# Performance work log

Hardware: AMD Instinct MI355X
Metric: run time of the kernel (lower is better)

## Reference

```python
import jax, jax.numpy as jnp
import numpy as np

INV_SQRT2 = 0.7071067811865476  # 1/sqrt(2), Haar / bior1.1 coefficient


def setup_inputs() -> dict:
    key = jax.random.key(0)
    ks = jax.random.split(key, 4)
    B, C, L = 8, 256, 4096
    s = 1.0 / np.sqrt(C).astype(np.float32)  # conv1d-style fan-in init scale
    return {
        "x": jax.random.normal(ks[0], (B, C, L), jnp.float32),
        "Wq": jax.random.normal(ks[1], (C, C), jnp.float32) * s,
        "bq": jnp.zeros((C,), jnp.float32),
        "Wk": jax.random.normal(ks[2], (C, C), jnp.float32) * s,
        "bk": jnp.zeros((C,), jnp.float32),
        "Wv": jax.random.normal(ks[3], (C, C), jnp.float32) * s,
        "bv": jnp.zeros((C,), jnp.float32),
        "attn_gate": jnp.full((1,), 0.5, jnp.float32),  # nonzero so gate path is exercised
    }


def reference(x, Wq, bq, Wk, bk, Wv, bv, attn_gate):
    # DWT1D(J=1, 'bior1.1', 'symmetric') high band; L even and filter len 2 => no padding.
    # pytorch_wavelets reverses pywt dec_hi=[-1,1]/sqrt2, so xh[i] = (x[2i]-x[2i+1])/sqrt2.
    xh = (x[..., 0::2] - x[..., 1::2]) * INV_SQRT2  # [B, C, L/2]

    # 1x1 conv projections == per-position linear over channels
    q = jnp.einsum('oc,bcl->bol', Wq, x) + bq[None, :, None]    # [B, C, L]
    k = jnp.einsum('oc,bcm->bom', Wk, xh) + bk[None, :, None]   # [B, C, L/2]
    v = jnp.einsum('oc,bcm->bom', Wv, xh) + bv[None, :, None]   # [B, C, L/2]

    scale = 1.0 / jnp.sqrt(jnp.asarray(q.shape[1], q.dtype))
    attn = jnp.einsum('bcm,bcl->bml', k, q) * scale  # [B, L/2, L] = K^T Q / sqrt(C)
    attn = jax.nn.softmax(attn, axis=1)              # softmax over the L/2 (key) axis
    yh = jnp.einsum('bcm,bml->bcl', v, attn)         # [B, C, L]

    return yh * jnp.tanh(attn_gate)[0] + x
```

## Files before the change

kernel.cpp:

```cpp
#include <hip/hip_runtime.h>
#include <hip/hip_bf16.h>

typedef __bf16 bf16_t;
typedef __bf16 bf16x8 __attribute__((ext_vector_type(8)));
typedef float  f32x2  __attribute__((ext_vector_type(2)));
typedef float  f32x4  __attribute__((ext_vector_type(4)));
typedef float  f32x16 __attribute__((ext_vector_type(16)));
typedef unsigned u32x2 __attribute__((ext_vector_type(2)));
typedef unsigned u32x4 __attribute__((ext_vector_type(4)));
typedef int    i32x8  __attribute__((ext_vector_type(8)));

#define B_ 8
#define C_ 256
#define L_ 4096
#define M_ 2048
#define INV_SQRT2f 0.70710678118654752440f
#define QSCALEf (0.0625f * 1.4426950408889634f)
#define EXP2R(x) __builtin_amdgcn_exp2f(x)

typedef __attribute__((address_space(3))) void as3_void;
typedef __attribute__((address_space(1))) const void as1_cvoid;

__device__ __forceinline__ void gload_lds16(const void* g, void* l) {
    __builtin_amdgcn_global_load_lds((as1_cvoid*)g, (as3_void*)l, 16, 0, 0);
}

__device__ __forceinline__ const bf16x8* ldg8(const bf16_t* p) {
    return reinterpret_cast<const bf16x8*>(p);
}

__device__ __forceinline__ unsigned packbf(float a, float b) {
    unsigned short ua = __builtin_bit_cast(unsigned short, (bf16_t)a);
    unsigned short ub = __builtin_bit_cast(unsigned short, (bf16_t)b);
    return (unsigned)ua | ((unsigned)ub << 16);
}

__device__ __forceinline__ void pl32swapu(unsigned &a, unsigned &b) {
    asm("v_permlane32_swap_b32 %0, %1" : "+v"(a), "+v"(b));
}

__device__ __forceinline__ int bs34(int v) {
    return (v & ~0x18) | ((v & 8) << 1) | ((v & 16) >> 1);
}

__device__ __forceinline__ unsigned pk4fp8(float a, float b, float c, float d) {
    int u = __builtin_amdgcn_cvt_pk_fp8_f32(a, b, 0, false);
    u = __builtin_amdgcn_cvt_pk_fp8_f32(c, d, u, true);
    return (unsigned)u;
}

__global__ __launch_bounds__(256) void conv_w_kernel(
    const float* __restrict__ Wq, const float* __restrict__ Wk, const float* __restrict__ Wv,
    bf16_t* __restrict__ Wqb, bf16_t* __restrict__ Wkb, bf16_t* __restrict__ Wvb) {
    int idx = blockIdx.x * 256 + threadIdx.x;
    int which = idx >> 16;
    int off = idx & 65535;
    const float* src = (which == 0) ? Wq : ((which == 1) ? Wk : Wv);
    bf16_t* dst = (which == 0) ? Wqb : ((which == 1) ? Wkb : Wvb);
    dst[off] = (bf16_t)src[off];
}

__global__ __launch_bounds__(256, 2) void kv_proj_kernel(
    const float* __restrict__ x, const bf16_t* __restrict__ Wk, const float* __restrict__ bk,
    const bf16_t* __restrict__ Wv, const float* __restrict__ bv,
    unsigned char* __restrict__ kb8, unsigned char* __restrict__ vb8) {
    __shared__ __align__(16) char smem[16384 + 33280];
    char* xh = smem;
    float* tile = (float*)(smem + 16384);

    const int t = threadIdx.x;
    const int wave = t >> 6, lane = t & 63;
    const int l31 = lane & 31, hi = lane >> 5;
    const int bid = blockIdx.x;
    const int b = bid & 7;
    const int mt = bid >> 3;
    const int m0 = mt * 32;

    const int c2 = (t & 31) * 2;
    const int mg = t >> 5;
    const int lrow = t >> 5;
    const int lcp  = t & 31;
    f32x2 stage[8];
    {
        const float* xs = x + ((size_t)(b * C_) * L_) + 2 * m0;
#pragma unroll
        for (int j = 0; j < 8; ++j)
            stage[j] = *reinterpret_cast<const f32x2*>(xs + (size_t)(lrow + 8 * j) * L_ + lcp * 2);
    }
    for (int cc = 0; cc < 4; ++cc) {
        if (cc) __syncthreads();
#pragma unroll
        for (int j = 0; j < 8; ++j)
            *reinterpret_cast<f32x2*>(tile + (lrow + 8 * j) * 130 + lcp * 2) = stage[j];
        __syncthreads();
        if (cc < 3) {
            const float* xs = x + ((size_t)(b * C_ + (cc + 1) * 64) * L_) + 2 * m0;
#pragma unroll
            for (int j = 0; j < 8; ++j)
                stage[j] = *reinterpret_cast<const f32x2*>(xs + (size_t)(lrow + 8 * j) * L_ + lcp * 2);
        }
#pragma unroll
        for (int i = 0; i < 4; ++i) {
            int m = mg * 4 + i;
            f32x2 pa = *reinterpret_cast<const f32x2*>(tile + c2 * 130 + 2 * m);
            f32x2 pb = *reinterpret_cast<const f32x2*>(tile + (c2 + 1) * 130 + 2 * m);
            float va  = (pa[0] - pa[1]) * INV_SQRT2f;
            float vb2 = (pb[0] - pb[1]) * INV_SQRT2f;
            int byte = m * 512 + ((((cc * 64 + c2) * 2)) ^ ((m & 7) << 4));
            *reinterpret_cast<unsigned*>(xh + byte) = packbf(va, vb2);
        }
    }
    __syncthreads();

    const int oq = wave;
    f32x16 kacc[2], vacc[2];
#pragma unroll
    for (int ob = 0; ob < 2; ++ob) {
        float bko = bk[(oq * 2 + ob) * 32 + l31];
#pragma unroll
        for (int r = 0; r < 16; ++r) { kacc[ob][r] = bko; vacc[ob][r] = 0.f; }
    }
    const int s0 = (l31 & 7) << 4;
#pragma unroll
    for (int ks = 0; ks < 16; ++ks) {
        int cb = (ks * 16 + hi * 8) * 2;
        bf16x8 xv = *reinterpret_cast<const bf16x8*>(xh + l31 * 512 + (cb ^ s0));
#pragma unroll
        for (int ob = 0; ob < 2; ++ob) {
            int o = (oq * 2 + ob) * 32 + l31;
            bf16x8 bw = *ldg8(Wk + (size_t)o * C_ + ks * 16 + hi * 8);
            kacc[ob] = __builtin_amdgcn_mfma_f32_32x32x16_bf16(xv, bw, kacc[ob], 0, 0, 0);
            bf16x8 aw = *ldg8(Wv + (size_t)o * C_ + ks * 16 + hi * 8);
            vacc[ob] = __builtin_amdgcn_mfma_f32_32x32x16_bf16(aw, xv, vacc[ob], 0, 0, 0);
        }
    }
    unsigned char* kout8 = kb8 + (size_t)b * M_ * C_;
    unsigned char* vout8 = vb8 + (size_t)b * C_ * M_;
#pragma unroll
    for (int ob = 0; ob < 2; ++ob) {
        int o = (oq * 2 + ob) * 32 + l31;
        int g = bs34(o);
#pragma unroll
        for (int r = 0; r < 16; ++r) {
            int mloc = (r & 3) + 8 * (r >> 2) + 4 * hi;
            unsigned p = (unsigned)__builtin_amdgcn_cvt_pk_fp8_f32(kacc[ob][r], kacc[ob][r], 0, false);
            kout8[(size_t)(m0 + mloc) * C_ + g] = (unsigned char)(p & 0xFF);
        }
#pragma unroll
        for (int r = 0; r < 16; ++r) {
            int ov = (oq * 2 + ob) * 32 + (r & 3) + 8 * (r >> 2) + 4 * hi;
            float val = vacc[ob][r] + bv[ov];
            unsigned p = (unsigned)__builtin_amdgcn_cvt_pk_fp8_f32(val, val, 0, false);
            vout8[(size_t)ov * M_ + m0 + l31] = (unsigned char)(p & 0xFF);
        }
    }
}

#define KT 64
#define NT (M_ / KT)

__global__ __launch_bounds__(512, 1) void attn_kernel(
    const bf16_t* __restrict__ Wq, const float* __restrict__ bq,
    const unsigned char* __restrict__ kb8, const unsigned char* __restrict__ vb8,
    const float* __restrict__ x, const float* __restrict__ gate, float* __restrict__ out) {
    __shared__ __align__(16) char smem[135168];
    char* Kbase_l = smem;
    float* tile   = (float*)(smem + 98304);

    const int t = threadIdx.x;
    const int wave = t >> 6, lane = t & 63;
    const int qg = wave & 3, mh = wave >> 2;
    const int l31 = lane & 31, hi = lane >> 5;
    const int bid = blockIdx.x;
    const int b = bid & 7;
    const int lt = bid >> 3;
    const int l0w = lt * 128 + qg * 32;

    i32x8 qfr[4];

    {
        char* xt = smem + 32768;
        const int cp2 = (t & 31) * 2;
        const int lg = t >> 5;
        const int lrow = t >> 6;
        const int lcp  = t & 63;
        f32x2 stage[8];
        {
            const float* xs = x + ((size_t)(b * C_) * L_) + lt * 128;
#pragma unroll
            for (int j = 0; j < 8; ++j)
                stage[j] = *reinterpret_cast<const f32x2*>(xs + (size_t)(lrow + 8 * j) * L_ + lcp * 2);
        }
        for (int cc = 0; cc < 4; ++cc) {
            if (cc) __syncthreads();
#pragma unroll
            for (int j = 0; j < 8; ++j)
                *reinterpret_cast<f32x2*>(tile + (lrow + 8 * j) * 130 + lcp * 2) = stage[j];
            __syncthreads();
            if (cc < 3) {
                const float* xs = x + ((size_t)(b * C_ + (cc + 1) * 64) * L_) + lt * 128;
#pragma unroll
                for (int j = 0; j < 8; ++j)
                    stage[j] = *reinterpret_cast<const f32x2*>(xs + (size_t)(lrow + 8 * j) * L_ + lcp * 2);
            }
#pragma unroll
            for (int i = 0; i < 8; ++i) {
                int l = lg * 8 + i;
                float va  = tile[cp2 * 130 + l];
                float vb2 = tile[(cp2 + 1) * 130 + l];
                int byte = l * 512 + ((((cc * 64 + cp2) * 2)) ^ ((l & 7) << 4));
                *reinterpret_cast<unsigned*>(xt + byte) = packbf(va, vb2);
            }
        }
        __syncthreads();

        const int ow = wave * 32;
        f32x16 qacc[4];
#pragma unroll
        for (int lb = 0; lb < 4; ++lb)
#pragma unroll
            for (int r = 0; r < 16; ++r) qacc[lb][r] = 0.f;
#pragma unroll
        for (int ks = 0; ks < 16; ++ks) {
            bf16x8 aw = *ldg8(Wq + (size_t)(ow + l31) * C_ + ks * 16 + hi * 8);
#pragma unroll
            for (int lb = 0; lb < 4; ++lb) {
                int lrow2 = lb * 32 + l31;
                bf16x8 bx = *reinterpret_cast<const bf16x8*>(
                    xt + lrow2 * 512 + (((ks * 16 + hi * 8) * 2) ^ ((lrow2 & 7) << 4)));
                qacc[lb] = __builtin_amdgcn_mfma_f32_32x32x16_bf16(aw, bx, qacc[lb], 0, 0, 0);
            }
        }
        char* qt = Kbase_l;
#pragma unroll
        for (int lb = 0; lb < 4; ++lb) {
            int l = lb * 32 + l31;
            int lsw = (l & 7) << 4;
#pragma unroll
            for (int q = 0; q < 4; ++q) {
                int o0 = ow + 4 * hi + 8 * q;
                f32x4 bq4 = *reinterpret_cast<const f32x4*>(bq + o0);
                unsigned w = pk4fp8((qacc[lb][q * 4 + 0] + bq4[0]) * QSCALEf,
                                    (qacc[lb][q * 4 + 1] + bq4[1]) * QSCALEf,
                                    (qacc[lb][q * 4 + 2] + bq4[2]) * QSCALEf,
                                    (qacc[lb][q * 4 + 3] + bq4[3]) * QSCALEf);
                int pos0 = bs34(o0);
                *reinterpret_cast<unsigned*>(qt + l * 256 + (pos0 ^ lsw)) = w;
            }
        }
        __syncthreads();
        const int qrow = qg * 32 + l31;
        const int qswz = (qrow & 7) << 4;
#pragma unroll
        for (int i = 0; i < 4; ++i) {
            u32x4 v0 = *reinterpret_cast<const u32x4*>(
                qt + qrow * 256 + (((2 * i) * 32 + hi * 16) ^ qswz));
            u32x4 v1 = *reinterpret_cast<const u32x4*>(
                qt + qrow * 256 + (((2 * i + 1) * 32 + hi * 16) ^ qswz));
            i32x8 q;
            q[0] = (int)v0[0]; q[1] = (int)v0[1]; q[2] = (int)v0[2]; q[3] = (int)v0[3];
            q[4] = (int)v1[0]; q[5] = (int)v1[1]; q[6] = (int)v1[2]; q[7] = (int)v1[3];
            qfr[i] = q;
        }
        __syncthreads();
    }

    const char* Kg = (const char*)(kb8 + (size_t)b * M_ * C_);
    int ksrc[2];
#pragma unroll
    for (int i = 0; i < 2; ++i) {
        int chunk = i * 8 + wave;
        int mr = chunk * 4 + (lane >> 4);
        ksrc[i] = mr * 256 + (((lane & 15) * 16) ^ ((mr & 7) << 4));
    }
    const int vrow = wave * 32 + (lane >> 1);
    const int vhalf = (lane & 1) * 32;
    const char* VgRow = (const char*)(vb8 + (size_t)b * C_ * M_ + (size_t)vrow * M_);
    const int vdoff = vrow * 72 + vhalf;

#pragma unroll
    for (int i = 0; i < 2; ++i)
        gload_lds16(Kg + ksrc[i], Kbase_l + (i * 8 + wave) * 1024);
    {
        u32x4 s0 = *reinterpret_cast<const u32x4*>(VgRow + vhalf);
        u32x4 s1 = *reinterpret_cast<const u32x4*>(VgRow + vhalf + 16);
        char* vd = smem + 32768 + vdoff;
        u32x2 w;
        w[0] = s0[0]; w[1] = s0[1]; *reinterpret_cast<u32x2*>(vd) = w;
        w[0] = s0[2]; w[1] = s0[3]; *reinterpret_cast<u32x2*>(vd + 8) = w;
        w[0] = s1[0]; w[1] = s1[1]; *reinterpret_cast<u32x2*>(vd + 16) = w;
        w[0] = s1[2]; w[1] = s1[3]; *reinterpret_cast<u32x2*>(vd + 24) = w;
    }

    f32x16 acc[8];
#pragma unroll
    for (int cb = 0; cb < 8; ++cb)
#pragma unroll
        for (int r = 0; r < 16; ++r) acc[cb][r] = 0.f;
    float m_run = -INFINITY, l_run = 0.f;

    asm volatile("s_waitcnt vmcnt(0) lgkmcnt(0)" ::: "memory");
    __builtin_amdgcn_s_barrier();
    asm volatile("" ::: "memory");

    for (int kt = 0; kt < NT; ++kt) {
        const int cur = kt & 1;
        u32x4 vstg0, vstg1;
        if (kt + 1 < NT) {
            const char* Kn = Kg + (size_t)(kt + 1) * 16384;
            char* Kd = Kbase_l + (cur ^ 1) * 16384;
#pragma unroll
            for (int i = 0; i < 2; ++i)
                gload_lds16(Kn + ksrc[i], Kd + (i * 8 + wave) * 1024);
            const char* src = VgRow + (size_t)(kt + 1) * 64 + vhalf;
            vstg0 = *reinterpret_cast<const u32x4*>(src);
            vstg1 = *reinterpret_cast<const u32x4*>(src + 16);
        }

        const char* Kc = Kbase_l + cur * 16384;
        const int mrow = mh * 32 + l31;
        const int msw = (mrow & 7) << 4;
        const int moff = mrow * 256;
        f32x16 s;
#pragma unroll
        for (int r = 0; r < 16; ++r) s[r] = 0.f;
        __builtin_amdgcn_s_setprio(1);
#pragma unroll
        for (int i = 0; i < 4; ++i) {
            u32x4 k0 = *reinterpret_cast<const u32x4*>(
                Kc + moff + (((2 * i) * 32 + hi * 16) ^ msw));
            u32x4 k1 = *reinterpret_cast<const u32x4*>(
                Kc + moff + (((2 * i + 1) * 32 + hi * 16) ^ msw));
            i32x8 a;
            a[0] = (int)k0[0]; a[1] = (int)k0[1]; a[2] = (int)k0[2]; a[3] = (int)k0[3];
            a[4] = (int)k1[0]; a[5] = (int)k1[1]; a[6] = (int)k1[2]; a[7] = (int)k1[3];
            s = __builtin_amdgcn_mfma_scale_f32_32x32x64_f8f6f4(
                    a, qfr[i], s, 0, 0, 0, 0x7F7F7F7F, 0, 0x7F7F7F7F);
        }
        __builtin_amdgcn_s_setprio(0);

        float pv[16];
        float tm = -INFINITY;
#pragma unroll
        for (int r = 0; r < 16; ++r) {
            pv[r] = s[r];
            tm = fmaxf(tm, s[r]);
        }
        tm = fmaxf(tm, __shfl_xor(tm, 32));
        if (!__all(tm - m_run <= 8.0f)) {
            float m_new = fmaxf(m_run, tm);
            float corr = EXP2R(m_run - m_new);
#pragma unroll
            for (int cb = 0; cb < 8; ++cb)
#pragma unroll
                for (int r = 0; r < 16; ++r) acc[cb][r] *= corr;
            l_run *= corr;
            m_run = m_new;
        }
        float rs = 0.f;
#pragma unroll
        for (int i = 0; i < 16; ++i) { pv[i] = EXP2R(pv[i] - m_run); rs += pv[i]; }
        l_run += rs;

        long pf0, pf1;
        {
            unsigned U0 = pk4fp8(pv[0], pv[1], pv[2], pv[3]);
            unsigned U1 = pk4fp8(pv[4], pv[5], pv[6], pv[7]);
            unsigned U2 = pk4fp8(pv[8], pv[9], pv[10], pv[11]);
            unsigned U3 = pk4fp8(pv[12], pv[13], pv[14], pv[15]);
            pl32swapu(U0, U1);
            pl32swapu(U2, U3);
            u32x2 p0; p0[0] = U0; p0[1] = U1;
            u32x2 p1; p1[0] = U2; p1[1] = U3;
            pf0 = __builtin_bit_cast(long, p0);
            pf1 = __builtin_bit_cast(long, p1);
        }

        const char* Vc = smem + 32768 + cur * 18432;
        __builtin_amdgcn_s_setprio(1);
#pragma unroll
        for (int ks2 = 0; ks2 < 2; ++ks2) {
            int mo = mh * 32 + ks2 * 16 + hi * 8;
            long pf = ks2 ? pf1 : pf0;
#pragma unroll
            for (int cb = 0; cb < 8; ++cb) {
                int c = cb * 32 + l31;
                long av = *reinterpret_cast<const long*>(Vc + c * 72 + mo);
                acc[cb] = __builtin_amdgcn_mfma_f32_32x32x16_fp8_fp8(av, pf, acc[cb], 0, 0, 0);
            }
        }
        __builtin_amdgcn_s_setprio(0);

        asm volatile("s_waitcnt vmcnt(0) lgkmcnt(0)" ::: "memory");
        if (kt + 1 < NT) {
            char* vd = smem + 32768 + (cur ^ 1) * 18432 + vdoff;
            u32x2 w;
            w[0] = vstg0[0]; w[1] = vstg0[1]; *reinterpret_cast<u32x2*>(vd) = w;
            w[0] = vstg0[2]; w[1] = vstg0[3]; *reinterpret_cast<u32x2*>(vd + 8) = w;
            w[0] = vstg1[0]; w[1] = vstg1[1]; *reinterpret_cast<u32x2*>(vd + 16) = w;
            w[0] = vstg1[2]; w[1] = vstg1[3]; *reinterpret_cast<u32x2*>(vd + 24) = w;
        }
        asm volatile("s_waitcnt lgkmcnt(0)" ::: "memory");
        __builtin_amdgcn_s_barrier();
        asm volatile("" ::: "memory");
    }

    l_run += __shfl_xor(l_run, 32);

    f32x2* mlb = (f32x2*)(smem + 131072);
    f32x2 myml; myml[0] = m_run; myml[1] = l_run;
    mlb[wave * 64 + lane] = myml;
    __syncthreads();
    f32x2 pml = mlb[(wave ^ 4) * 64 + lane];
    float m_star = fmaxf(m_run, pml[0]);
    float f_self = EXP2R(m_run - m_star);
    float f_peer = EXP2R(pml[0] - m_star);
    float l_tot = l_run * f_self + pml[1] * f_peer;
#pragma unroll
    for (int cb = 0; cb < 8; ++cb)
#pragma unroll
        for (int r = 0; r < 16; ++r) acc[cb][r] *= f_self;

    char* xbuf = smem;
    const int myoff = (qg * 2 + mh) * 16384;
    __syncthreads();
#pragma unroll
    for (int cbl = 0; cbl < 4; ++cbl)
#pragma unroll
        for (int q = 0; q < 4; ++q) {
            f32x4 chunk;
#pragma unroll
            for (int j = 0; j < 4; ++j) {
                float a_lo = acc[cbl][q * 4 + j];
                float a_hi = acc[4 + cbl][q * 4 + j];
                chunk[j] = mh ? a_lo : a_hi;
            }
            *reinterpret_cast<f32x4*>(xbuf + myoff + (cbl * 4 + q) * 1024 + lane * 16) = chunk;
        }
    __syncthreads();

    const int poff = (qg * 2 + (1 - mh)) * 16384;
    float gt = tanhf(gate[0]);
    float scale = gt / l_tot;
    const float* xp = x + (size_t)b * C_ * L_;
    float* op = out + (size_t)b * C_ * L_;
    int lcol = l0w + l31;
    const int cbase = mh * 4;
#pragma unroll
    for (int cbl = 0; cbl < 4; ++cbl) {
#pragma unroll
        for (int q = 0; q < 4; ++q) {
            f32x4 pc = *reinterpret_cast<const f32x4*>(xbuf + poff + (cbl * 4 + q) * 1024 + lane * 16);
#pragma unroll
            for (int j = 0; j < 4; ++j) {
                float a_lo = acc[cbl][q * 4 + j];
                float a_hi = acc[4 + cbl][q * 4 + j];
                float mine = mh ? a_hi : a_lo;
                int c = (cbase + cbl) * 32 + j + 8 * q + 4 * hi;
                size_t idx = (size_t)c * L_ + lcol;
                op[idx] = (mine + pc[j]) * scale + xp[idx];
            }
        }
    }
}

extern "C" void kernel_launch(void* const* d_in, const int* in_sizes, int n_in,
                              void* d_out, int out_size, void* d_ws, size_t ws_size,
                              hipStream_t stream) {
    const float* x    = (const float*)d_in[0];
    const float* Wq   = (const float*)d_in[1];
    const float* bq   = (const float*)d_in[2];
    const float* Wk   = (const float*)d_in[3];
    const float* bk   = (const float*)d_in[4];
    const float* Wv   = (const float*)d_in[5];
    const float* bv   = (const float*)d_in[6];
    const float* gate = (const float*)d_in[7];
    float* out = (float*)d_out;

    char* ws = (char*)d_ws;
    const size_t szK8 = (size_t)B_ * M_ * C_;
    const size_t szV8 = (size_t)B_ * M_ * C_;
    const size_t szW  = (size_t)C_ * C_ * 2;
    unsigned char* kbuf8 = (unsigned char*)(ws);
    unsigned char* vbuf8 = (unsigned char*)(ws + szK8);
    bf16_t* Wqb  = (bf16_t*)(ws + szK8 + szV8);
    bf16_t* Wkb  = (bf16_t*)(ws + szK8 + szV8 + szW);
    bf16_t* Wvb  = (bf16_t*)(ws + szK8 + szV8 + 2 * szW);

    conv_w_kernel<<<768, 256, 0, stream>>>(Wq, Wk, Wv, Wqb, Wkb, Wvb);
    kv_proj_kernel<<<512, 256, 0, stream>>>(x, Wkb, bk, Wvb, bv, kbuf8, vbuf8);
    attn_kernel<<<256, 512, 0, stream>>>(Wqb, bq, kbuf8, vbuf8, x, gate, out);
}
```

Before: 97.08 us.

## Halve attention block to 64 queries with 4 waves, two blocks per CU

Restructures the attention kernel from 512-thread blocks covering 128 query positions into 256-thread blocks covering 64 positions, launching 512 blocks with launch bounds allowing two per CU. LDS use drops to about 68KB so two blocks can co-reside. Work distribution changes across the kernel: Q projection now gives each wave 64 output channels, K loads use 4 chunks per wave, and each thread stages a full 64-byte V row. The aim is better latency hiding and finer scheduling across CUs. In exchange, K/V tiles are streamed from memory twice as often overall, and the Q projection is split into more, smaller blocks.

```diff
diff --git a/kernel.cpp b/kernel.cpp
--- a/kernel.cpp
+++ b/kernel.cpp
@@ -159,34 +159,36 @@
 #define KT 64
 #define NT (M_ / KT)
 
-__global__ __launch_bounds__(512, 1) void attn_kernel(
+__global__ __launch_bounds__(256, 2) void attn_kernel(
     const bf16_t* __restrict__ Wq, const float* __restrict__ bq,
     const unsigned char* __restrict__ kb8, const unsigned char* __restrict__ vb8,
     const float* __restrict__ x, const float* __restrict__ gate, float* __restrict__ out) {
-    __shared__ __align__(16) char smem[135168];
+    __shared__ __align__(16) char smem[69632];
     char* Kbase_l = smem;
-    float* tile   = (float*)(smem + 98304);
+    char* Vbuf    = smem + 32768;
 
     const int t = threadIdx.x;
     const int wave = t >> 6, lane = t & 63;
-    const int qg = wave & 3, mh = wave >> 2;
+    const int qg = wave & 1, mh = wave >> 1;
     const int l31 = lane & 31, hi = lane >> 5;
     const int bid = blockIdx.x;
     const int b = bid & 7;
     const int lt = bid >> 3;
-    const int l0w = lt * 128 + qg * 32;
+    const int l0w = lt * 64 + qg * 32;
 
     i32x8 qfr[4];
 
     {
-        char* xt = smem + 32768;
+        char* qt = smem;
+        char* xt = smem + 16384;
+        float* tile = (float*)(smem + 49152);
         const int cp2 = (t & 31) * 2;
         const int lg = t >> 5;
-        const int lrow = t >> 6;
-        const int lcp  = t & 63;
+        const int lrow = t >> 5;
+        const int lcp  = t & 31;
         f32x2 stage[8];
         {
-            const float* xs = x + ((size_t)(b * C_) * L_) + lt * 128;
+            const float* xs = x + ((size_t)(b * C_) * L_) + lt * 64;
 #pragma unroll
             for (int j = 0; j < 8; ++j)
                 stage[j] = *reinterpret_cast<const f32x2*>(xs + (size_t)(lrow + 8 * j) * L_ + lcp * 2);
@@ -195,10 +197,10 @@
             if (cc) __syncthreads();
 #pragma unroll
             for (int j = 0; j < 8; ++j)
-                *reinterpret_cast<f32x2*>(tile + (lrow + 8 * j) * 130 + lcp * 2) = stage[j];
+                *reinterpret_cast<f32x2*>(tile + (lrow + 8 * j) * 66 + lcp * 2) = stage[j];
             __syncthreads();
             if (cc < 3) {
-                const float* xs = x + ((size_t)(b * C_ + (cc + 1) * 64) * L_) + lt * 128;
+                const float* xs = x + ((size_t)(b * C_ + (cc + 1) * 64) * L_) + lt * 64;
 #pragma unroll
                 for (int j = 0; j < 8; ++j)
                     stage[j] = *reinterpret_cast<const f32x2*>(xs + (size_t)(lrow + 8 * j) * L_ + lcp * 2);
@@ -206,48 +208,52 @@
 #pragma unroll
             for (int i = 0; i < 8; ++i) {
                 int l = lg * 8 + i;
-                float va  = tile[cp2 * 130 + l];
-                float vb2 = tile[(cp2 + 1) * 130 + l];
+                float va  = tile[cp2 * 66 + l];
+                float vb2 = tile[(cp2 + 1) * 66 + l];
                 int byte = l * 512 + ((((cc * 64 + cp2) * 2)) ^ ((l & 7) << 4));
                 *reinterpret_cast<unsigned*>(xt + byte) = packbf(va, vb2);
             }
         }
         __syncthreads();
 
-        const int ow = wave * 32;
         f32x16 qacc[4];
 #pragma unroll
-        for (int lb = 0; lb < 4; ++lb)
-#pragma unroll
-            for (int r = 0; r < 16; ++r) qacc[lb][r] = 0.f;
+        for (int i2 = 0; i2 < 4; ++i2)
+#pragma unroll
+            for (int r = 0; r < 16; ++r) qacc[i2][r] = 0.f;
 #pragma unroll
         for (int ks = 0; ks < 16; ++ks) {
-            bf16x8 aw = *ldg8(Wq + (size_t)(ow + l31) * C_ + ks * 16 + hi * 8);
-#pragma unroll
-            for (int lb = 0; lb < 4; ++lb) {
-                int lrow2 = lb * 32 + l31;
-                bf16x8 bx = *reinterpret_cast<const bf16x8*>(
-                    xt + lrow2 * 512 + (((ks * 16 + hi * 8) * 2) ^ ((lrow2 & 7) << 4)));
-                qacc[lb] = __builtin_amdgcn_mfma_f32_32x32x16_bf16(aw, bx, qacc[lb], 0, 0, 0);
-            }
-        }
-        char* qt = Kbase_l;
-#pragma unroll
-        for (int lb = 0; lb < 4; ++lb) {
-            int l = lb * 32 + l31;
-            int lsw = (l & 7) << 4;
-#pragma unroll
-            for (int q = 0; q < 4; ++q) {
-                int o0 = ow + 4 * hi + 8 * q;
-                f32x4 bq4 = *reinterpret_cast<const f32x4*>(bq + o0);
-                unsigned w = pk4fp8((qacc[lb][q * 4 + 0] + bq4[0]) * QSCALEf,
-                                    (qacc[lb][q * 4 + 1] + bq4[1]) * QSCALEf,
-                                    (qacc[lb][q * 4 + 2] + bq4[2]) * QSCALEf,
-                                    (qacc[lb][q * 4 + 3] + bq4[3]) * QSCALEf);
-                int pos0 = bs34(o0);
-                *reinterpret_cast<unsigned*>(qt + l * 256 + (pos0 ^ lsw)) = w;
-            }
-        }
+#pragma unroll
+            for (int ob = 0; ob < 2; ++ob) {
+                bf16x8 aw = *ldg8(Wq + (size_t)(wave * 64 + ob * 32 + l31) * C_ + ks * 16 + hi * 8);
+#pragma unroll
+                for (int lb = 0; lb < 2; ++lb) {
+                    int lrow2 = lb * 32 + l31;
+                    bf16x8 bx = *reinterpret_cast<const bf16x8*>(
+                        xt + lrow2 * 512 + (((ks * 16 + hi * 8) * 2) ^ ((lrow2 & 7) << 4)));
+                    qacc[ob * 2 + lb] = __builtin_amdgcn_mfma_f32_32x32x16_bf16(aw, bx, qacc[ob * 2 + lb], 0, 0, 0);
+                }
+            }
+        }
+        __syncthreads();
+#pragma unroll
+        for (int ob = 0; ob < 2; ++ob)
+#pragma unroll
+            for (int lb = 0; lb < 2; ++lb) {
+                int l = lb * 32 + l31;
+                int lsw = (l & 7) << 4;
+#pragma unroll
+                for (int q = 0; q < 4; ++q) {
+                    int o0 = wave * 64 + ob * 32 + 4 * hi + 8 * q;
+                    f32x4 bq4 = *reinterpret_cast<const f32x4*>(bq + o0);
+                    unsigned w = pk4fp8((qacc[ob * 2 + lb][q * 4 + 0] + bq4[0]) * QSCALEf,
+                                        (qacc[ob * 2 + lb][q * 4 + 1] + bq4[1]) * QSCALEf,
+                                        (qacc[ob * 2 + lb][q * 4 + 2] + bq4[2]) * QSCALEf,
+                                        (qacc[ob * 2 + lb][q * 4 + 3] + bq4[3]) * QSCALEf);
+                    int pos0 = bs34(o0);
+                    *reinterpret_cast<unsigned*>(qt + l * 256 + (pos0 ^ lsw)) = w;
+                }
+            }
         __syncthreads();
         const int qrow = qg * 32 + l31;
         const int qswz = (qrow & 7) << 4;
@@ -266,30 +272,34 @@
     }
 
     const char* Kg = (const char*)(kb8 + (size_t)b * M_ * C_);
-    int ksrc[2];
-#pragma unroll
-    for (int i = 0; i < 2; ++i) {
-        int chunk = i * 8 + wave;
+    int ksrc[4];
+#pragma unroll
+    for (int i = 0; i < 4; ++i) {
+        int chunk = i * 4 + wave;
         int mr = chunk * 4 + (lane >> 4);
         ksrc[i] = mr * 256 + (((lane & 15) * 16) ^ ((mr & 7) << 4));
     }
-    const int vrow = wave * 32 + (lane >> 1);
-    const int vhalf = (lane & 1) * 32;
-    const char* VgRow = (const char*)(vb8 + (size_t)b * C_ * M_ + (size_t)vrow * M_);
-    const int vdoff = vrow * 72 + vhalf;
-
-#pragma unroll
-    for (int i = 0; i < 2; ++i)
-        gload_lds16(Kg + ksrc[i], Kbase_l + (i * 8 + wave) * 1024);
+    const char* VgRow = (const char*)(vb8 + (size_t)b * C_ * M_ + (size_t)t * M_);
+    const int vdoff = t * 72;
+
+#pragma unroll
+    for (int i = 0; i < 4; ++i)
+        gload_lds16(Kg + ksrc[i], Kbase_l + (i * 4 + wave) * 1024);
     {
-        u32x4 s0 = *reinterpret_cast<const u32x4*>(VgRow + vhalf);
-        u32x4 s1 = *reinterpret_cast<const u32x4*>(VgRow + vhalf + 16);
-        char* vd = smem + 32768 + vdoff;
+        u32x4 s0 = *reinterpret_cast<const u32x4*>(VgRow);
+        u32x4 s1 = *reinterpret_cast<const u32x4*>(VgRow + 16);
+        u32x4 s2 = *reinterpret_cast<const u32x4*>(VgRow + 32);
+        u32x4 s3 = *reinterpret_cast<const u32x4*>(VgRow + 48);
+        char* vd = Vbuf + vdoff;
         u32x2 w;
         w[0] = s0[0]; w[1] = s0[1]; *reinterpret_cast<u32x2*>(vd) = w;
         w[0] = s0[2]; w[1] = s0[3]; *reinterpret_cast<u32x2*>(vd + 8) = w;
         w[0] = s1[0]; w[1] = s1[1]; *reinterpret_cast<u32x2*>(vd + 16) = w;
         w[0] = s1[2]; w[1] = s1[3]; *reinterpret_cast<u32x2*>(vd + 24) = w;
+        w[0] = s2[0]; w[1] = s2[1]; *reinterpret_cast<u32x2*>(vd + 32) = w;
+        w[0] = s2[2]; w[1] = s2[3]; *reinterpret_cast<u32x2*>(vd + 40) = w;
+        w[0] = s3[0]; w[1] = s3[1]; *reinterpret_cast<u32x2*>(vd + 48) = w;
+        w[0] = s3[2]; w[1] = s3[3]; *reinterpret_cast<u32x2*>(vd + 56) = w;
     }
 
     f32x16 acc[8];
@@ -305,16 +315,18 @@
 
     for (int kt = 0; kt < NT; ++kt) {
         const int cur = kt & 1;
-        u32x4 vstg0, vstg1;
+        u32x4 vstg0, vstg1, vstg2, vstg3;
         if (kt + 1 < NT) {
             const char* Kn = Kg + (size_t)(kt + 1) * 16384;
             char* Kd = Kbase_l + (cur ^ 1) * 16384;
 #pragma unroll
-            for (int i = 0; i < 2; ++i)
-                gload_lds16(Kn + ksrc[i], Kd + (i * 8 + wave) * 1024);
-            const char* src = VgRow + (size_t)(kt + 1) * 64 + vhalf;
+            for (int i = 0; i < 4; ++i)
+                gload_lds16(Kn + ksrc[i], Kd + (i * 4 + wave) * 1024);
+            const char* src = VgRow + (size_t)(kt + 1) * 64;
             vstg0 = *reinterpret_cast<const u32x4*>(src);
             vstg1 = *reinterpret_cast<const u32x4*>(src + 16);
+            vstg2 = *reinterpret_cast<const u32x4*>(src + 32);
+            vstg3 = *reinterpret_cast<const u32x4*>(src + 48);
         }
 
         const char* Kc = Kbase_l + cur * 16384;
@@ -376,7 +388,7 @@
             pf1 = __builtin_bit_cast(long, p1);
         }
 
-        const char* Vc = smem + 32768 + cur * 18432;
+        const char* Vc = Vbuf + cur * 18432;
         __builtin_amdgcn_s_setprio(1);
 #pragma unroll
         for (int ks2 = 0; ks2 < 2; ++ks2) {
@@ -393,12 +405,16 @@
 
         asm volatile("s_waitcnt vmcnt(0) lgkmcnt(0)" ::: "memory");
         if (kt + 1 < NT) {
-            char* vd = smem + 32768 + (cur ^ 1) * 18432 + vdoff;
+            char* vd = Vbuf + (cur ^ 1) * 18432 + vdoff;
             u32x2 w;
             w[0] = vstg0[0]; w[1] = vstg0[1]; *reinterpret_cast<u32x2*>(vd) = w;
             w[0] = vstg0[2]; w[1] = vstg0[3]; *reinterpret_cast<u32x2*>(vd + 8) = w;
             w[0] = vstg1[0]; w[1] = vstg1[1]; *reinterpret_cast<u32x2*>(vd + 16) = w;
             w[0] = vstg1[2]; w[1] = vstg1[3]; *reinterpret_cast<u32x2*>(vd + 24) = w;
+            w[0] = vstg2[0]; w[1] = vstg2[1]; *reinterpret_cast<u32x2*>(vd + 32) = w;
+            w[0] = vstg2[2]; w[1] = vstg2[3]; *reinterpret_cast<u32x2*>(vd + 40) = w;
+            w[0] = vstg3[0]; w[1] = vstg3[1]; *reinterpret_cast<u32x2*>(vd + 48) = w;
+            w[0] = vstg3[2]; w[1] = vstg3[3]; *reinterpret_cast<u32x2*>(vd + 56) = w;
         }
         asm volatile("s_waitcnt lgkmcnt(0)" ::: "memory");
         __builtin_amdgcn_s_barrier();
@@ -407,11 +423,11 @@
 
     l_run += __shfl_xor(l_run, 32);
 
-    f32x2* mlb = (f32x2*)(smem + 131072);
+    f32x2* mlb = (f32x2*)(smem + 67584);
     f32x2 myml; myml[0] = m_run; myml[1] = l_run;
     mlb[wave * 64 + lane] = myml;
     __syncthreads();
-    f32x2 pml = mlb[(wave ^ 4) * 64 + lane];
+    f32x2 pml = mlb[(wave ^ 2) * 64 + lane];
     float m_star = fmaxf(m_run, pml[0]);
     float f_self = EXP2R(m_run - m_star);
     float f_peer = EXP2R(pml[0] - m_star);
@@ -489,5 +505,5 @@
 
     conv_w_kernel<<<768, 256, 0, stream>>>(Wq, Wk, Wv, Wqb, Wkb, Wvb);
     kv_proj_kernel<<<512, 256, 0, stream>>>(x, Wkb, bk, Wvb, bv, kbuf8, vbuf8);
-    attn_kernel<<<256, 512, 0, stream>>>(Wqb, bq, kbuf8, vbuf8, x, gate, out);
-}
+    attn_kernel<<<512, 256, 0, stream>>>(Wqb, bq, kbuf8, vbuf8, x, gate, out);
+}
```

Result: slower. 104.3 us (+7.4%).
